# Optimization experiments

Hardware: AMD Instinct MI355X
Metric: run time of the kernel (lower is better)

Reference implementation:

```python
import jax, jax.numpy as jnp
import numpy as np

EPS = 1e-5
K = 3

def _bn(x, g, b):
    # training-mode BatchNorm2d: batch stats over (N,H,W), biased variance
    m = jnp.mean(x, axis=(0, 2, 3), keepdims=True)
    v = jnp.var(x, axis=(0, 2, 3), keepdims=True)
    return (x - m) * jax.lax.rsqrt(v + EPS) * g[None, :, None, None] + b[None, :, None, None]

def _gelu(x):
    return jax.nn.gelu(x, approximate=False)

def _dyn_dw(x, aw1, ab1, aw2, ab2):
    # dynamic depthwise conv: per-sample k^2 softmax weights shared over channels
    b, c, h, w = x.shape
    gap = jnp.mean(x, axis=(2, 3))                              # (b,c)
    h1 = jax.nn.relu(jnp.einsum('oc,bc->bo', aw1, gap) + ab1)   # (b,c//8)
    kw = jax.nn.softmax(jnp.einsum('oc,bc->bo', aw2, h1) + ab2, axis=1)  # (b,k^2)
    xp = jnp.pad(x, ((0, 0), (0, 0), (1, 1), (1, 1)))
    out = jnp.zeros_like(x)
    idx = 0
    for i in range(K):
        for j in range(K):
            out = out + kw[:, idx, None, None, None] * xp[:, :, i:i + h, j:j + w]
            idx += 1
    return out

def _channel_att(x, w1, w2):
    avg = jnp.mean(x, axis=(2, 3))        # (b,C)
    mx = jnp.max(x, axis=(2, 3))          # (b,C)
    def fc(v):
        return jnp.einsum('oc,bc->bo', w2, jax.nn.relu(jnp.einsum('oc,bc->bo', w1, v)))
    s = jax.nn.sigmoid(fc(avg) + fc(mx))  # (b,C)
    return s[:, :, None, None] * x

def _forward(x, w1, b1, g1, be1, aw1, ab1, aw2, ab2, g2, be2,
             ca_w1, ca_w2, pw, pb, g3, be3, sw, sb):
    b, n, d = x.shape
    h = w = int(np.sqrt(n))
    residual = x
    xi = jnp.transpose(x.reshape(b, h, w, d), (0, 3, 1, 2))       # (b,d,h,w)
    # pw_expand: 1x1 conv -> GELU -> BN
    y = jnp.einsum('oc,bchw->bohw', w1, xi) + b1[None, :, None, None]
    y = _bn(_gelu(y), g1, be1)                                    # (b,4d,h,w)
    # dw_conv: dynamic depthwise -> GELU -> BN -> channel attention
    y = _dyn_dw(y, aw1, ab1, aw2, ab2)
    y = _bn(_gelu(y), g2, be2)
    y = _channel_att(y, ca_w1, ca_w2)
    # spatial attention
    avg_o = jnp.mean(y, axis=1, keepdims=True)
    max_o = jnp.max(y, axis=1, keepdims=True)
    sp_in = jnp.concatenate([avg_o, max_o], axis=1)               # (b,2,h,w)
    sp = jax.lax.conv_general_dilated(sp_in, sw, (1, 1), ((3, 3), (3, 3)),
                                      dimension_numbers=('NCHW', 'OIHW', 'NCHW'))
    sp = jax.nn.sigmoid(sp + sb[None, :, None, None])
    y = y * sp
    # pw_project: 1x1 conv -> BN
    y = jnp.einsum('oc,bchw->bohw', pw, y) + pb[None, :, None, None]
    y = _bn(y, g3, be3)
    y = jnp.transpose(y, (0, 2, 3, 1)).reshape(b, n, d)
    return residual + y

def setup_inputs() -> dict:
    key = jax.random.key(0)
    ks = jax.random.split(key, 16)
    d, C = 256, 1024
    def rn(k, shape, fan):
        return jax.random.normal(k, shape, jnp.float32) * np.float32(np.sqrt(2.0 / fan))
    return {
        'x': jax.random.normal(ks[0], (8, 1024, d), jnp.float32),
        'w1': rn(ks[1], (C, d), d), 'b1': jnp.zeros((C,), jnp.float32),
        'g1': jnp.ones((C,), jnp.float32), 'be1': jnp.zeros((C,), jnp.float32),
        'aw1': rn(ks[2], (C // 8, C), C), 'ab1': jnp.zeros((C // 8,), jnp.float32),
        'aw2': rn(ks[3], (K * K, C // 8), C // 8), 'ab2': jnp.zeros((K * K,), jnp.float32),
        'g2': jnp.ones((C,), jnp.float32), 'be2': jnp.zeros((C,), jnp.float32),
        'ca_w1': rn(ks[4], (C // 16, C), C), 'ca_w2': rn(ks[5], (C, C // 16), C // 16),
        'pw': rn(ks[6], (d, C), C), 'pb': jnp.zeros((d,), jnp.float32),
        'g3': jnp.ones((d,), jnp.float32), 'be3': jnp.zeros((d,), jnp.float32),
        'sw': rn(ks[7], (1, 2, 7, 7), 2 * 49), 'sb': jnp.zeros((1,), jnp.float32),
    }

def reference(x, w1, b1, g1, be1, aw1, ab1, aw2, ab2, g2, be2,
              ca_w1, ca_w2, pw, pb, g3, be3, sw, sb):
    return _forward(x, w1, b1, g1, be1, aw1, ab1, aw2, ab2, g2, be2,
                    ca_w1, ca_w2, pw, pb, g3, be3, sw, sb)
```

## Files before the change

### kernel.cpp

```cpp
#include <hip/hip_runtime.h>
#include <math.h>

constexpr int B = 8;
constexpr int D = 256;
constexpr int C = 1024;
constexpr int H = 32, W = 32;
constexpr int P = H * W;
constexpr int M = B * P;
constexpr float EPS = 1e-5f;

typedef unsigned short u16;
typedef unsigned int u32;
typedef __attribute__((ext_vector_type(8))) short short8;
typedef __attribute__((ext_vector_type(4))) float floatx4;

constexpr size_t WS_CHSUM1 = 0;
constexpr size_t WS_CHSQ1  = 1024;
constexpr size_t WS_GAPSUM = 2048;
constexpr size_t WS_CHSUM3 = 10240;
constexpr size_t WS_CHSQ3  = 10496;
constexpr size_t WS_CHSUM2 = 10752;
constexpr size_t WS_CHSQ2  = 11776;
constexpr size_t WS_BSUM2  = 12800;
constexpr size_t WS_UMAX2  = 20992;
constexpr size_t WS_UMAXN2 = 29184;
constexpr size_t WS_ACC_COUNT = 37376;
constexpr size_t WS_SCALE1 = 37376;
constexpr size_t WS_SHIFT1 = 38400;
constexpr size_t WS_KW     = 39424;
constexpr size_t WS_SCALE2 = 39680;
constexpr size_t WS_SHIFT2 = 40704;
constexpr size_t WS_SATT   = 41728;
constexpr size_t WS_AVGO   = 49920;
constexpr size_t WS_MAXO   = 58112;
constexpr size_t WS_SP     = 66304;
constexpr size_t WS_PRE    = 74496;
constexpr size_t WS_T1B    = 2171648;
constexpr size_t WS_T2B    = 6365952;
constexpr size_t WS_XB     = 10560256;
constexpr size_t WS_W1B    = 11608832;
constexpr size_t WS_PWB    = 11739904;
constexpr size_t WS_YB     = 11870976;

__device__ __forceinline__ float gelu_exact(float v) {
    return 0.5f * v * (1.0f + erff(v * 0.70710678118654752440f));
}

__device__ __forceinline__ u16 f2bf(float f) {
    u32 u = __float_as_uint(f);
    u += 0x7fff + ((u >> 16) & 1);
    return (u16)(u >> 16);
}

__device__ __forceinline__ float bf2f(u16 v) {
    return __uint_as_float(((u32)v) << 16);
}

__device__ __forceinline__ u32 fkey(float f) {
    u32 u = __float_as_uint(f);
    return (u & 0x80000000u) ? ~u : (u | 0x80000000u);
}
__device__ __forceinline__ float fkeyinv(u32 k) {
    return __uint_as_float((k & 0x80000000u) ? (k ^ 0x80000000u) : ~k);
}

#define GLOAD(SRC, DST) __builtin_amdgcn_global_load_lds( \
    (const __attribute__((address_space(1))) void*)(SRC), \
    (__attribute__((address_space(3))) void*)(DST), 16, 0, 0)

__global__ __launch_bounds__(256) void cvt_all_kernel(const float* __restrict__ x,
                                                      const float* __restrict__ w1,
                                                      const float* __restrict__ pw,
                                                      u16* __restrict__ xb,
                                                      u16* __restrict__ w1b,
                                                      u16* __restrict__ pwb,
                                                      float* __restrict__ acc_zero) {
    const int i = blockIdx.x * 256 + threadIdx.x;
    if (i < (int)WS_ACC_COUNT) acc_zero[i] = 0.f;
    const float* src;
    u16* dst;
    int off;
    if (i < 524288)      { src = x;  dst = xb;  off = i; }
    else if (i < 589824) { src = w1; dst = w1b; off = i - 524288; }
    else                 { src = pw; dst = pwb; off = i - 589824; }
    const float4 v = *(const float4*)(src + (size_t)off * 4);
    uint2 o;
    o.x = ((u32)f2bf(v.x)) | ((u32)f2bf(v.y) << 16);
    o.y = ((u32)f2bf(v.z)) | ((u32)f2bf(v.w) << 16);
    *(uint2*)(dst + (size_t)off * 4) = o;
}

template<int KD, int EPI, int NS, int MB, int NB>
__global__ __launch_bounds__(256) void mfma_gemm_kernel(
    const u16* __restrict__ A,
    const u16* __restrict__ Bw,
    const float* __restrict__ bias,
    const float* __restrict__ rowscale,
    void* __restrict__ outv,
    float* __restrict__ csum,
    float* __restrict__ csq,
    float* __restrict__ gsum)
{
    constexpr int MI = MB / 32;
    constexpr int NJ = NB / 32;
    constexpr int ABUF = MB * 32;
    constexpr int BBUF = NB * 32;
    constexpr int BUFSZ = ABUF + BBUF;
    constexpr int GA = MB / 64;
    constexpr int GB = NB / 64;
    constexpr int LD = GA + GB;
    constexpr int NCH = KD / 32;
    constexpr int GX = NS / NB;
    constexpr int NWG = (M / MB) * GX;
    constexpr int CPX = NWG / 8;
    extern __shared__ u16 smem[];
    const int t = threadIdx.x;
    const int lane = t & 63;

    const int lin = blockIdx.y * GX + blockIdx.x;
    const int swz = (lin & 7) * CPX + (lin >> 3);
    const int bx = swz % GX;
    const int by = swz / GX;
    const int row0 = by * MB;
    const int col0 = bx * NB;

    const int wv = t >> 6;
    const int wrow = (wv >> 1) * (MB / 2);
    const int wcol = (wv & 1) * (NB / 2);
    const int lm = lane & 15;
    const int lk8 = (lane >> 4) * 8;
    const int srow = t >> 2;
    const int scol = (t & 3) * 8;
    const u16* gA = A + (size_t)(row0 + srow) * KD + scol;
    const u16* gB = Bw + (size_t)(col0 + srow) * KD + scol;

    const floatx4 zero = {0.f, 0.f, 0.f, 0.f};
    floatx4 acc[MI][NJ];
#pragma unroll
    for (int i = 0; i < MI; ++i)
#pragma unroll
        for (int j = 0; j < NJ; ++j) acc[i][j] = zero;

    auto stage = [&](u16* buf, int c) {
        const int kk = c * 32;
        u16* As = buf;
        u16* Bs = buf + ABUF;
#pragma unroll
        for (int g = 0; g < GA; ++g)
            GLOAD(gA + (size_t)g * 64 * KD + kk, As + g * 2048 + t * 8);
#pragma unroll
        for (int g = 0; g < GB; ++g)
            GLOAD(gB + (size_t)g * 64 * KD + kk, Bs + g * 2048 + t * 8);
    };
    auto compute = [&](const u16* buf) {
        const u16* As = buf;
        const u16* Bs = buf + ABUF;
        short8 af[MI], bf[NJ];
#pragma unroll
        for (int i = 0; i < MI; ++i)
            af[i] = *(const short8*)(As + (wrow + i * 16 + lm) * 32 + lk8);
#pragma unroll
        for (int j = 0; j < NJ; ++j)
            bf[j] = *(const short8*)(Bs + (wcol + j * 16 + lm) * 32 + lk8);
#pragma unroll
        for (int i = 0; i < MI; ++i)
#pragma unroll
            for (int j = 0; j < NJ; ++j)
                acc[i][j] = __builtin_amdgcn_mfma_f32_16x16x32_bf16(af[i], bf[j], acc[i][j], 0, 0, 0);
    };

    stage(smem, 0);
    for (int c = 0; c < NCH; ++c) {
        u16* curb = smem + (c & 1) * BUFSZ;
        if (c + 1 < NCH) {
            stage(smem + ((c + 1) & 1) * BUFSZ, c + 1);
            if constexpr (LD == 2) asm volatile("s_waitcnt vmcnt(2)" ::: "memory");
            else                   asm volatile("s_waitcnt vmcnt(3)" ::: "memory");
        } else {
            asm volatile("s_waitcnt vmcnt(0)" ::: "memory");
        }
        __builtin_amdgcn_s_barrier();
        compute(curb);
        asm volatile("s_waitcnt lgkmcnt(0)" ::: "memory");
        __builtin_amdgcn_s_barrier();
    }

    float colsum[NJ], colsq[NJ];
#pragma unroll
    for (int j = 0; j < NJ; ++j) { colsum[j] = 0.f; colsq[j] = 0.f; }

    if (EPI == 0) {
        u16* Cs = smem;
#pragma unroll
        for (int i = 0; i < MI; ++i) {
#pragma unroll
            for (int r = 0; r < 4; ++r) {
                const int lrow = wrow + i * 16 + (lane >> 4) * 4 + r;
#pragma unroll
                for (int j = 0; j < NJ; ++j) {
                    const int lcol = wcol + j * 16 + lm;
                    const float tv = gelu_exact(acc[i][j][r] + bias[col0 + lcol]);
                    Cs[lrow * NB + lcol] = f2bf(tv);
                    colsum[j] += tv;
                    colsq[j] = fmaf(tv, tv, colsq[j]);
                }
            }
        }
        __syncthreads();
        constexpr int TPR = NB / 8;
        constexpr int RPP = 256 / TPR;
        u16* outp = (u16*)outv;
#pragma unroll
        for (int p = 0; p < MB / RPP; ++p) {
            const int r = p * RPP + t / TPR;
            const int cc = (t % TPR) * 8;
            *(uint4*)(outp + (size_t)(row0 + r) * NS + col0 + cc) =
                *(const uint4*)(Cs + r * NB + cc);
        }
    } else {
        float* Cs = (float*)smem;
#pragma unroll
        for (int i = 0; i < MI; ++i) {
#pragma unroll
            for (int r = 0; r < 4; ++r) {
                const int lrow = wrow + i * 16 + (lane >> 4) * 4 + r;
                const float rs = rowscale[row0 + lrow];
#pragma unroll
                for (int j = 0; j < NJ; ++j) {
                    const int lcol = wcol + j * 16 + lm;
                    const float tv = rs * acc[i][j][r] + bias[col0 + lcol];
                    Cs[lrow * NB + lcol] = tv;
                    colsum[j] += tv;
                    colsq[j] = fmaf(tv, tv, colsq[j]);
                }
            }
        }
        __syncthreads();
        constexpr int TPR = NB / 4;
        constexpr int RPP = 256 / TPR;
        float* outp = (float*)outv;
#pragma unroll
        for (int p = 0; p < MB / RPP; ++p) {
            const int r = p * RPP + t / TPR;
            const int cc = (t % TPR) * 4;
            *(float4*)(outp + (size_t)(row0 + r) * NS + col0 + cc) =
                *(const float4*)(Cs + r * NB + cc);
        }
    }

    const int bb = (by * MB) >> 10;
#pragma unroll
    for (int j = 0; j < NJ; ++j) {
        float s = colsum[j];
        float q = colsq[j];
        s += __shfl_xor(s, 16); s += __shfl_xor(s, 32);
        q += __shfl_xor(q, 16); q += __shfl_xor(q, 32);
        if (lane < 16) {
            const int c = col0 + wcol + j * 16 + lm;
            atomicAdd(&csum[c], s);
            atomicAdd(&csq[c], q);
            if (EPI == 0) atomicAdd(&gsum[bb * NS + c], s);
        }
    }
}

__global__ __launch_bounds__(1024) void dynmlp_kernel(const float* __restrict__ chsum1,
                                                      const float* __restrict__ chsq1,
                                                      const float* __restrict__ gapsum,
                                                      const float* __restrict__ g1,
                                                      const float* __restrict__ be1,
                                                      const float* __restrict__ aw1,
                                                      const float* __restrict__ ab1,
                                                      const float* __restrict__ aw2,
                                                      const float* __restrict__ ab2,
                                                      float* __restrict__ scale1,
                                                      float* __restrict__ shift1,
                                                      float* __restrict__ kw) {
    const int b = blockIdx.x;
    const int t = threadIdx.x;
    const int wave = t >> 6, lane = t & 63;
    __shared__ float g[1024];
    __shared__ float h1[128];
    __shared__ float logits[12];
    {
        const float m = chsum1[t] * (1.0f / (float)M);
        const float var = chsq1[t] * (1.0f / (float)M) - m * m;
        const float rstd = rsqrtf(var + EPS);
        const float sc = rstd * g1[t];
        const float sh = be1[t] - m * sc;
        if (b == 0) { scale1[t] = sc; shift1[t] = sh; }
        g[t] = gapsum[b * C + t] * (1.0f / (float)P) * sc + sh;
    }
    __syncthreads();
#pragma unroll
    for (int k = 0; k < 8; ++k) {
        const int u = wave * 8 + k;
        const float4* wr = (const float4*)(aw1 + (size_t)u * C);
        float s = 0.f;
#pragma unroll
        for (int ch = 0; ch < 4; ++ch) {
            const float4 wv = wr[lane + 64 * ch];
            const float4 sv = *(const float4*)(g + 4 * lane + 256 * ch);
            s += wv.x * sv.x + wv.y * sv.y + wv.z * sv.z + wv.w * sv.w;
        }
#pragma unroll
        for (int off = 1; off < 64; off <<= 1) s += __shfl_xor(s, off);
        if (lane == 0) h1[u] = fmaxf(s + ab1[u], 0.f);
    }
    __syncthreads();
    if (wave < 9) {
        float s = aw2[wave * 128 + lane] * h1[lane]
                + aw2[wave * 128 + 64 + lane] * h1[64 + lane];
#pragma unroll
        for (int off = 1; off < 64; off <<= 1) s += __shfl_xor(s, off);
        if (lane == 0) logits[wave] = s + ab2[wave];
    }
    __syncthreads();
    if (t == 0) {
        float mx = logits[0];
        for (int i = 1; i < 9; ++i) mx = fmaxf(mx, logits[i]);
        float e[9], den = 0.f;
        for (int i = 0; i < 9; ++i) { e[i] = expf(logits[i] - mx); den += e[i]; }
        const float inv = 1.0f / den;
        for (int i = 0; i < 9; ++i) kw[b * 9 + i] = e[i] * inv;
    }
}

__global__ __launch_bounds__(256) void dwconv_kernel(const u16* __restrict__ t1b,
                                                     const float* __restrict__ scale1,
                                                     const float* __restrict__ shift1,
                                                     const float* __restrict__ kw,
                                                     u16* __restrict__ t2b,
                                                     float* __restrict__ chsum2,
                                                     float* __restrict__ chsq2,
                                                     float* __restrict__ bsum2,
                                                     u32* __restrict__ umax2,
                                                     u32* __restrict__ umaxn2) {
    __shared__ u16 rows[3 * 32 * 256];
    const int lin = blockIdx.y * 4 + blockIdx.x;
    const int swz = (lin & 7) * 128 + (lin >> 3);
    const int cq = swz & 3;
    const int bh = swz >> 2;
    const int b = bh >> 5;
    const int h = bh & 31;
    const int t = threadIdx.x;

    const u16* gbase = t1b + (size_t)b * P * C + cq * 256;
#pragma unroll
    for (int i = 0; i < 12; ++i) {
        const int lin2 = i * 256 + t;
        const int chunk = lin2 >> 5;
        const int r = chunk >> 5;
        const int w = chunk & 31;
        const int off8 = (lin2 & 31) * 8;
        const int hr = h + r - 1;
        uint4 v = {0u, 0u, 0u, 0u};
        if (hr >= 0 && hr < H)
            v = *(const uint4*)(gbase + (size_t)(hr * W + w) * C + off8);
        *(uint4*)(&rows[chunk * 256 + off8]) = v;
    }
    __syncthreads();

    const int c = t;
    const int gc = cq * 256 + c;
    float kk[9];
#pragma unroll
    for (int i = 0; i < 9; ++i) kk[i] = kw[b * 9 + i];
    const float sc = scale1[gc];
    const float sh = shift1[gc];
    float scm[3], shm[3];
    scm[0] = (h > 0)     ? sc : 0.f;  shm[0] = (h > 0)     ? sh : 0.f;
    scm[1] = sc;                      shm[1] = sh;
    scm[2] = (h < H - 1) ? sc : 0.f;  shm[2] = (h < H - 1) ? sh : 0.f;

    const u16* rp0 = rows + c;
#define DWVAL(ri, w) fmaf(bf2f(rp0[((ri) * 32 + (w)) * 256]), scm[ri], shm[ri])

    float vm0 = 0.f, vm1 = 0.f, vm2 = 0.f;
    float vc0 = DWVAL(0, 0), vc1 = DWVAL(1, 0), vc2 = DWVAL(2, 0);
    float vp0 = DWVAL(0, 1), vp1 = DWVAL(1, 1), vp2 = DWVAL(2, 1);

    float s = 0.f, q = 0.f, mx = -INFINITY, mn = INFINITY;
    u16* orow = t2b + ((size_t)b * P + h * W) * C + gc;
    for (int w = 0; w < W; ++w) {
        float acc;
        acc = kk[0] * vm0;
        acc = fmaf(kk[1], vc0, acc);
        acc = fmaf(kk[2], vp0, acc);
        acc = fmaf(kk[3], vm1, acc);
        acc = fmaf(kk[4], vc1, acc);
        acc = fmaf(kk[5], vp1, acc);
        acc = fmaf(kk[6], vm2, acc);
        acc = fmaf(kk[7], vc2, acc);
        acc = fmaf(kk[8], vp2, acc);
        const float y = gelu_exact(acc);
        orow[(size_t)w * C] = f2bf(y);
        s += y;
        q = fmaf(y, y, q);
        mx = fmaxf(mx, y);
        mn = fminf(mn, y);
        vm0 = vc0; vc0 = vp0;
        vm1 = vc1; vc1 = vp1;
        vm2 = vc2; vc2 = vp2;
        if (w + 2 < W) {
            vp0 = DWVAL(0, w + 2);
            vp1 = DWVAL(1, w + 2);
            vp2 = DWVAL(2, w + 2);
        } else {
            vp0 = 0.f; vp1 = 0.f; vp2 = 0.f;
        }
    }
#undef DWVAL
    atomicAdd(&chsum2[gc], s);
    atomicAdd(&chsq2[gc], q);
    atomicAdd(&bsum2[b * C + gc], s);
    atomicMax(&umax2[b * C + gc], fkey(mx));
    atomicMax(&umaxn2[b * C + gc], fkey(-mn));
}

__global__ __launch_bounds__(1024) void chatt_kernel(const float* __restrict__ chsum2,
                                                     const float* __restrict__ chsq2,
                                                     const float* __restrict__ bsum2,
                                                     const u32* __restrict__ umax2,
                                                     const u32* __restrict__ umaxn2,
                                                     const float* __restrict__ g2,
                                                     const float* __restrict__ be2,
                                                     const float* __restrict__ caw1,
                                                     const float* __restrict__ caw2,
                                                     float* __restrict__ scale2,
                                                     float* __restrict__ shift2,
                                                     float* __restrict__ s_att) {
    const int b = blockIdx.x;
    const int t = threadIdx.x;
    const int wave = t >> 6, lane = t & 63;
    __shared__ float la[1024], lx[1024], ha[64], hm[64];
    {
        const float m = chsum2[t] * (1.0f / (float)M);
        const float var = chsq2[t] * (1.0f / (float)M) - m * m;
        const float rstd = rsqrtf(var + EPS);
        const float sc = rstd * g2[t];
        const float sh = be2[t] - m * sc;
        if (b == 0) { scale2[t] = sc; shift2[t] = sh; }
        la[t] = bsum2[b * C + t] * (1.0f / (float)P) * sc + sh;
        const float mx = fkeyinv(umax2[b * C + t]);
        const float mn = -fkeyinv(umaxn2[b * C + t]);
        lx[t] = (sc >= 0.f ? mx : mn) * sc + sh;
    }
    __syncthreads();
#pragma unroll
    for (int k = 0; k < 8; ++k) {
        const int u = wave * 8 + k;
        const int row = u & 63;
        const float* src = (u < 64) ? la : lx;
        const float4* wr = (const float4*)(caw1 + (size_t)row * C);
        float s = 0.f;
#pragma unroll
        for (int ch = 0; ch < 4; ++ch) {
            const float4 wv = wr[lane + 64 * ch];
            const float4 sv = *(const float4*)(src + 4 * lane + 256 * ch);
            s += wv.x * sv.x + wv.y * sv.y + wv.z * sv.z + wv.w * sv.w;
        }
#pragma unroll
        for (int off = 1; off < 64; off <<= 1) s += __shfl_xor(s, off);
        if (lane == 0) {
            s = fmaxf(s, 0.f);
            if (u < 64) ha[row] = s; else hm[row] = s;
        }
    }
    __syncthreads();
    {
        const float4* w2 = (const float4*)(caw2 + (size_t)t * 64);
        float s = 0.f;
#pragma unroll
        for (int j = 0; j < 16; ++j) {
            const float4 wv = w2[j];
            s += wv.x * (ha[j * 4 + 0] + hm[j * 4 + 0]);
            s += wv.y * (ha[j * 4 + 1] + hm[j * 4 + 1]);
            s += wv.z * (ha[j * 4 + 2] + hm[j * 4 + 2]);
            s += wv.w * (ha[j * 4 + 3] + hm[j * 4 + 3]);
        }
        s_att[b * C + t] = 1.0f / (1.0f + expf(-s));
    }
}

__global__ __launch_bounds__(256) void yq_kernel(const u16* __restrict__ t2b,
                                                 const float* __restrict__ scale2,
                                                 const float* __restrict__ shift2,
                                                 const float* __restrict__ s_att,
                                                 u16* __restrict__ yb,
                                                 float* __restrict__ avg_o,
                                                 float* __restrict__ max_o) {
    const int row = blockIdx.x;
    const int b = row >> 10;
    const int t = threadIdx.x;
    const int c0 = t * 4;
    const uint2 vv = *(const uint2*)(t2b + (size_t)row * C + c0);
    const float v0 = bf2f((u16)(vv.x & 0xffff));
    const float v1 = bf2f((u16)(vv.x >> 16));
    const float v2 = bf2f((u16)(vv.y & 0xffff));
    const float v3 = bf2f((u16)(vv.y >> 16));
    const float4 sc = *(const float4*)(scale2 + c0);
    const float4 sh = *(const float4*)(shift2 + c0);
    const float4 sa = *(const float4*)(s_att + (size_t)b * C + c0);
    const float y0 = fmaf(v0, sc.x, sh.x) * sa.x;
    const float y1 = fmaf(v1, sc.y, sh.y) * sa.y;
    const float y2 = fmaf(v2, sc.z, sh.z) * sa.z;
    const float y3 = fmaf(v3, sc.w, sh.w) * sa.w;
    uint2 o;
    o.x = ((u32)f2bf(y0)) | ((u32)f2bf(y1) << 16);
    o.y = ((u32)f2bf(y2)) | ((u32)f2bf(y3) << 16);
    *(uint2*)(yb + (size_t)row * C + c0) = o;
    float s = (y0 + y1) + (y2 + y3);
    float mx = fmaxf(fmaxf(y0, y1), fmaxf(y2, y3));
#pragma unroll
    for (int off = 32; off > 0; off >>= 1) {
        s += __shfl_down(s, off);
        mx = fmaxf(mx, __shfl_down(mx, off));
    }
    __shared__ float ss[4], sm[4];
    const int wave = t >> 6, lane = t & 63;
    if (lane == 0) { ss[wave] = s; sm[wave] = mx; }
    __syncthreads();
    if (t == 0) {
        const float S = ss[0] + ss[1] + ss[2] + ss[3];
        const float Mx = fmaxf(fmaxf(sm[0], sm[1]), fmaxf(sm[2], sm[3]));
        avg_o[row] = S * (1.0f / (float)C);
        max_o[row] = Mx;
    }
}

__global__ __launch_bounds__(1024) void spconv_kernel(const float* __restrict__ avg_o,
                                                      const float* __restrict__ max_o,
                                                      const float* __restrict__ sw,
                                                      const float* __restrict__ sb,
                                                      float* __restrict__ sp) {
    const int b = blockIdx.x;
    const int t = threadIdx.x;
    __shared__ float pa[P], pm[P], wsh[98];
    pa[t] = avg_o[b * P + t];
    pm[t] = max_o[b * P + t];
    if (t < 98) wsh[t] = sw[t];
    const float sbv = sb[0];
    __syncthreads();
    const int h = t >> 5, w = t & 31;
    float acc = sbv;
#pragma unroll
    for (int i = 0; i < 7; ++i) {
        const int hh = h + i - 3;
        if (hh < 0 || hh >= H) continue;
#pragma unroll
        for (int j = 0; j < 7; ++j) {
            const int ww = w + j - 3;
            if (ww < 0 || ww >= W) continue;
            const int pidx = hh * W + ww;
            acc = fmaf(wsh[i * 7 + j], pa[pidx], acc);
            acc = fmaf(wsh[49 + i * 7 + j], pm[pidx], acc);
        }
    }
    sp[b * P + t] = 1.0f / (1.0f + expf(-acc));
}

__global__ __launch_bounds__(256) void final_kernel(const float* __restrict__ x,
                                                    const float* __restrict__ pre,
                                                    const float* __restrict__ chsum3,
                                                    const float* __restrict__ chsq3,
                                                    const float* __restrict__ g3,
                                                    const float* __restrict__ be3,
                                                    float* __restrict__ out) {
    __shared__ float lsc[256], lsh[256];
    const int t = threadIdx.x;
    {
        const float m = chsum3[t] * (1.0f / (float)M);
        const float var = chsq3[t] * (1.0f / (float)M) - m * m;
        const float rstd = rsqrtf(var + EPS);
        const float sc = rstd * g3[t];
        lsc[t] = sc;
        lsh[t] = be3[t] - m * sc;
    }
    __syncthreads();
    const int i = blockIdx.x * 256 + t;
    const int e = i * 4;
    const int d = e & 255;
    const float4 xv = *(const float4*)(x + e);
    const float4 pv = *(const float4*)(pre + e);
    const float4 sc = *(const float4*)(lsc + d);
    const float4 sh = *(const float4*)(lsh + d);
    float4 o;
    o.x = xv.x + fmaf(pv.x, sc.x, sh.x);
    o.y = xv.y + fmaf(pv.y, sc.y, sh.y);
    o.z = xv.z + fmaf(pv.z, sc.z, sh.z);
    o.w = xv.w + fmaf(pv.w, sc.w, sh.w);
    *(float4*)(out + e) = o;
}

extern "C" void kernel_launch(void* const* d_in, const int* in_sizes, int n_in,
                              void* d_out, int out_size, void* d_ws, size_t ws_size,
                              hipStream_t stream) {
    const float* x    = (const float*)d_in[0];
    const float* w1   = (const float*)d_in[1];
    const float* b1   = (const float*)d_in[2];
    const float* g1   = (const float*)d_in[3];
    const float* be1  = (const float*)d_in[4];
    const float* aw1  = (const float*)d_in[5];
    const float* ab1  = (const float*)d_in[6];
    const float* aw2  = (const float*)d_in[7];
    const float* ab2  = (const float*)d_in[8];
    const float* g2   = (const float*)d_in[9];
    const float* be2  = (const float*)d_in[10];
    const float* caw1 = (const float*)d_in[11];
    const float* caw2 = (const float*)d_in[12];
    const float* pw   = (const float*)d_in[13];
    const float* pb   = (const float*)d_in[14];
    const float* g3   = (const float*)d_in[15];
    const float* be3  = (const float*)d_in[16];
    const float* sw   = (const float*)d_in[17];
    const float* sb   = (const float*)d_in[18];
    float* out = (float*)d_out;
    float* ws = (float*)d_ws;

    float* chsum1  = ws + WS_CHSUM1;
    float* chsq1   = ws + WS_CHSQ1;
    float* gapsum  = ws + WS_GAPSUM;
    float* chsum3  = ws + WS_CHSUM3;
    float* chsq3   = ws + WS_CHSQ3;
    float* chsum2  = ws + WS_CHSUM2;
    float* chsq2   = ws + WS_CHSQ2;
    float* bsum2   = ws + WS_BSUM2;
    u32*   umax2   = (u32*)(ws + WS_UMAX2);
    u32*   umaxn2  = (u32*)(ws + WS_UMAXN2);
    float* scale1  = ws + WS_SCALE1;
    float* shift1  = ws + WS_SHIFT1;
    float* kw      = ws + WS_KW;
    float* scale2  = ws + WS_SCALE2;
    float* shift2  = ws + WS_SHIFT2;
    float* s_att   = ws + WS_SATT;
    float* avg_o   = ws + WS_AVGO;
    float* max_o   = ws + WS_MAXO;
    float* sp      = ws + WS_SP;
    float* pre     = ws + WS_PRE;
    u16* t1b = (u16*)(ws + WS_T1B);
    u16* t2b = (u16*)(ws + WS_T2B);
    u16* xb  = (u16*)(ws + WS_XB);
    u16* w1b = (u16*)(ws + WS_W1B);
    u16* pwb = (u16*)(ws + WS_PWB);
    u16* yb  = (u16*)(ws + WS_YB);

    cvt_all_kernel<<<dim3(2560), 256, 0, stream>>>(x, w1, pw, xb, w1b, pwb, ws);
    mfma_gemm_kernel<256, 0, C, 128, 64><<<dim3(C / 64, M / 128), 256, 24576, stream>>>(
        xb, w1b, b1, nullptr, t1b, chsum1, chsq1, gapsum);
    dynmlp_kernel<<<dim3(B), 1024, 0, stream>>>(chsum1, chsq1, gapsum, g1, be1,
                                                aw1, ab1, aw2, ab2, scale1, shift1, kw);
    dwconv_kernel<<<dim3(4, B * H), 256, 0, stream>>>(t1b, scale1, shift1, kw, t2b,
                                                      chsum2, chsq2, bsum2, umax2, umaxn2);
    chatt_kernel<<<dim3(B), 1024, 0, stream>>>(chsum2, chsq2, bsum2, umax2, umaxn2,
                                               g2, be2, caw1, caw2, scale2, shift2, s_att);
    yq_kernel<<<dim3(M), 256, 0, stream>>>(t2b, scale2, shift2, s_att, yb, avg_o, max_o);
    spconv_kernel<<<dim3(B), 1024, 0, stream>>>(avg_o, max_o, sw, sb, sp);
    mfma_gemm_kernel<1024, 1, D, 64, 64><<<dim3(D / 64, M / 64), 256, 16384, stream>>>(
        yb, pwb, pb, sp, pre, chsum3, chsq3, nullptr);
    final_kernel<<<dim3((M * D / 4) / 256), 256, 0, stream>>>(x, pre, chsum3, chsq3, g3, be3, out);
}
```

Baseline: 202.8 us.

## Fold BN2 and channel attention into per-batch projection weights, drop yb materialization

```diff
diff --git a/kernel.cpp b/kernel.cpp
--- a/kernel.cpp
+++ b/kernel.cpp
@@ -40,7 +40,8 @@
 constexpr size_t WS_XB     = 10560256;
 constexpr size_t WS_W1B    = 11608832;
 constexpr size_t WS_PWB    = 11739904;
-constexpr size_t WS_YB     = 11870976;
+constexpr size_t WS_PWBF   = 11870976;
+constexpr size_t WS_BIAS2  = 12919552;
 
 __device__ __forceinline__ float gelu_exact(float v) {
     return 0.5f * v * (1.0f + erff(v * 0.70710678118654752440f));
@@ -70,19 +71,16 @@
 
 __global__ __launch_bounds__(256) void cvt_all_kernel(const float* __restrict__ x,
                                                       const float* __restrict__ w1,
-                                                      const float* __restrict__ pw,
                                                       u16* __restrict__ xb,
                                                       u16* __restrict__ w1b,
-                                                      u16* __restrict__ pwb,
                                                       float* __restrict__ acc_zero) {
     const int i = blockIdx.x * 256 + threadIdx.x;
     if (i < (int)WS_ACC_COUNT) acc_zero[i] = 0.f;
     const float* src;
     u16* dst;
     int off;
-    if (i < 524288)      { src = x;  dst = xb;  off = i; }
-    else if (i < 589824) { src = w1; dst = w1b; off = i - 524288; }
-    else                 { src = pw; dst = pwb; off = i - 589824; }
+    if (i < 524288) { src = x;  dst = xb;  off = i; }
+    else            { src = w1; dst = w1b; off = i - 524288; }
     const float4 v = *(const float4*)(src + (size_t)off * 4);
     uint2 o;
     o.x = ((u32)f2bf(v.x)) | ((u32)f2bf(v.y) << 16);
@@ -123,6 +121,7 @@
     const int by = swz / GX;
     const int row0 = by * MB;
     const int col0 = bx * NB;
+    const int bb = row0 >> 10;
 
     const int wv = t >> 6;
     const int wrow = (wv >> 1) * (MB / 2);
@@ -132,7 +131,9 @@
     const int srow = t >> 2;
     const int scol = (t & 3) * 8;
     const u16* gA = A + (size_t)(row0 + srow) * KD + scol;
-    const u16* gB = Bw + (size_t)(col0 + srow) * KD + scol;
+    const u16* gB = Bw + (EPI == 1 ? (size_t)bb * NS * KD : (size_t)0)
+                       + (size_t)(col0 + srow) * KD + scol;
+    const float* biasp = bias + (EPI == 1 ? bb * NS : 0);
 
     const floatx4 zero = {0.f, 0.f, 0.f, 0.f};
     floatx4 acc[MI][NJ];
@@ -199,7 +200,7 @@
 #pragma unroll
                 for (int j = 0; j < NJ; ++j) {
                     const int lcol = wcol + j * 16 + lm;
-                    const float tv = gelu_exact(acc[i][j][r] + bias[col0 + lcol]);
+                    const float tv = gelu_exact(acc[i][j][r] + biasp[col0 + lcol]);
                     Cs[lrow * NB + lcol] = f2bf(tv);
                     colsum[j] += tv;
                     colsq[j] = fmaf(tv, tv, colsq[j]);
@@ -211,8 +212,8 @@
         constexpr int RPP = 256 / TPR;
         u16* outp = (u16*)outv;
 #pragma unroll
-        for (int p = 0; p < MB / RPP; ++p) {
-            const int r = p * RPP + t / TPR;
+        for (int pp = 0; pp < MB / RPP; ++pp) {
+            const int r = pp * RPP + t / TPR;
             const int cc = (t % TPR) * 8;
             *(uint4*)(outp + (size_t)(row0 + r) * NS + col0 + cc) =
                 *(const uint4*)(Cs + r * NB + cc);
@@ -228,7 +229,7 @@
 #pragma unroll
                 for (int j = 0; j < NJ; ++j) {
                     const int lcol = wcol + j * 16 + lm;
-                    const float tv = rs * acc[i][j][r] + bias[col0 + lcol];
+                    const float tv = rs * (acc[i][j][r] + biasp[col0 + lcol]);
                     Cs[lrow * NB + lcol] = tv;
                     colsum[j] += tv;
                     colsq[j] = fmaf(tv, tv, colsq[j]);
@@ -240,15 +241,14 @@
         constexpr int RPP = 256 / TPR;
         float* outp = (float*)outv;
 #pragma unroll
-        for (int p = 0; p < MB / RPP; ++p) {
-            const int r = p * RPP + t / TPR;
+        for (int pp = 0; pp < MB / RPP; ++pp) {
+            const int r = pp * RPP + t / TPR;
             const int cc = (t % TPR) * 4;
             *(float4*)(outp + (size_t)(row0 + r) * NS + col0 + cc) =
                 *(const float4*)(Cs + r * NB + cc);
         }
     }
 
-    const int bb = (by * MB) >> 10;
 #pragma unroll
     for (int j = 0; j < NJ; ++j) {
         float s = colsum[j];
@@ -427,19 +427,24 @@
                                                      const float* __restrict__ be2,
                                                      const float* __restrict__ caw1,
                                                      const float* __restrict__ caw2,
+                                                     const float* __restrict__ pw,
+                                                     const float* __restrict__ pb,
                                                      float* __restrict__ scale2,
                                                      float* __restrict__ shift2,
-                                                     float* __restrict__ s_att) {
+                                                     float* __restrict__ s_att,
+                                                     u16* __restrict__ pwb,
+                                                     float* __restrict__ bias2) {
     const int b = blockIdx.x;
     const int t = threadIdx.x;
     const int wave = t >> 6, lane = t & 63;
     __shared__ float la[1024], lx[1024], ha[64], hm[64];
+    float sc, sh;
     {
         const float m = chsum2[t] * (1.0f / (float)M);
         const float var = chsq2[t] * (1.0f / (float)M) - m * m;
         const float rstd = rsqrtf(var + EPS);
-        const float sc = rstd * g2[t];
-        const float sh = be2[t] - m * sc;
+        sc = rstd * g2[t];
+        sh = be2[t] - m * sc;
         if (b == 0) { scale2[t] = sc; shift2[t] = sh; }
         la[t] = bsum2[b * C + t] * (1.0f / (float)P) * sc + sh;
         const float mx = fkeyinv(umax2[b * C + t]);
@@ -468,6 +473,7 @@
         }
     }
     __syncthreads();
+    float sat;
     {
         const float4* w2 = (const float4*)(caw2 + (size_t)t * 64);
         float s = 0.f;
@@ -479,7 +485,32 @@
             s += wv.z * (ha[j * 4 + 2] + hm[j * 4 + 2]);
             s += wv.w * (ha[j * 4 + 3] + hm[j * 4 + 3]);
         }
-        s_att[b * C + t] = 1.0f / (1.0f + expf(-s));
+        sat = 1.0f / (1.0f + expf(-s));
+        s_att[b * C + t] = sat;
+    }
+    __syncthreads();
+    la[t] = sc * sat;
+    lx[t] = sh * sat;
+    __syncthreads();
+    {
+        const int d = t >> 2;
+        const int cbase = (t & 3) * 256;
+        const float* pwr = pw + (size_t)d * C + cbase;
+        u16* pwbr = pwb + ((size_t)b * D + d) * C + cbase;
+        float bacc = 0.f;
+        for (int i = 0; i < 256; i += 4) {
+            const float4 wv = *(const float4*)(pwr + i);
+            const float4 f1 = *(const float4*)(la + cbase + i);
+            const float4 f2 = *(const float4*)(lx + cbase + i);
+            uint2 o;
+            o.x = ((u32)f2bf(wv.x * f1.x)) | ((u32)f2bf(wv.y * f1.y) << 16);
+            o.y = ((u32)f2bf(wv.z * f1.z)) | ((u32)f2bf(wv.w * f1.w) << 16);
+            *(uint2*)(pwbr + i) = o;
+            bacc += wv.x * f2.x + wv.y * f2.y + wv.z * f2.z + wv.w * f2.w;
+        }
+        bacc += __shfl_xor(bacc, 1);
+        bacc += __shfl_xor(bacc, 2);
+        if ((t & 3) == 0) bias2[b * D + d] = pb[d] + bacc;
     }
 }
 
@@ -487,7 +518,6 @@
                                                  const float* __restrict__ scale2,
                                                  const float* __restrict__ shift2,
                                                  const float* __restrict__ s_att,
-                                                 u16* __restrict__ yb,
                                                  float* __restrict__ avg_o,
                                                  float* __restrict__ max_o) {
     const int row = blockIdx.x;
@@ -506,10 +536,6 @@
     const float y1 = fmaf(v1, sc.y, sh.y) * sa.y;
     const float y2 = fmaf(v2, sc.z, sh.z) * sa.z;
     const float y3 = fmaf(v3, sc.w, sh.w) * sa.w;
-    uint2 o;
-    o.x = ((u32)f2bf(y0)) | ((u32)f2bf(y1) << 16);
-    o.y = ((u32)f2bf(y2)) | ((u32)f2bf(y3) << 16);
-    *(uint2*)(yb + (size_t)row * C + c0) = o;
     float s = (y0 + y1) + (y2 + y3);
     float mx = fmaxf(fmaxf(y0, y1), fmaxf(y2, y3));
 #pragma unroll
@@ -638,14 +664,14 @@
     float* max_o   = ws + WS_MAXO;
     float* sp      = ws + WS_SP;
     float* pre     = ws + WS_PRE;
-    u16* t1b = (u16*)(ws + WS_T1B);
-    u16* t2b = (u16*)(ws + WS_T2B);
-    u16* xb  = (u16*)(ws + WS_XB);
-    u16* w1b = (u16*)(ws + WS_W1B);
-    u16* pwb = (u16*)(ws + WS_PWB);
-    u16* yb  = (u16*)(ws + WS_YB);
-
-    cvt_all_kernel<<<dim3(2560), 256, 0, stream>>>(x, w1, pw, xb, w1b, pwb, ws);
+    float* bias2   = ws + WS_BIAS2;
+    u16* t1b  = (u16*)(ws + WS_T1B);
+    u16* t2b  = (u16*)(ws + WS_T2B);
+    u16* xb   = (u16*)(ws + WS_XB);
+    u16* w1b  = (u16*)(ws + WS_W1B);
+    u16* pwbf = (u16*)(ws + WS_PWBF);
+
+    cvt_all_kernel<<<dim3(2304), 256, 0, stream>>>(x, w1, xb, w1b, ws);
     mfma_gemm_kernel<256, 0, C, 128, 64><<<dim3(C / 64, M / 128), 256, 24576, stream>>>(
         xb, w1b, b1, nullptr, t1b, chsum1, chsq1, gapsum);
     dynmlp_kernel<<<dim3(B), 1024, 0, stream>>>(chsum1, chsq1, gapsum, g1, be1,
@@ -653,10 +679,11 @@
     dwconv_kernel<<<dim3(4, B * H), 256, 0, stream>>>(t1b, scale1, shift1, kw, t2b,
                                                       chsum2, chsq2, bsum2, umax2, umaxn2);
     chatt_kernel<<<dim3(B), 1024, 0, stream>>>(chsum2, chsq2, bsum2, umax2, umaxn2,
-                                               g2, be2, caw1, caw2, scale2, shift2, s_att);
-    yq_kernel<<<dim3(M), 256, 0, stream>>>(t2b, scale2, shift2, s_att, yb, avg_o, max_o);
+                                               g2, be2, caw1, caw2, pw, pb,
+                                               scale2, shift2, s_att, pwbf, bias2);
+    yq_kernel<<<dim3(M), 256, 0, stream>>>(t2b, scale2, shift2, s_att, avg_o, max_o);
     spconv_kernel<<<dim3(B), 1024, 0, stream>>>(avg_o, max_o, sw, sb, sp);
-    mfma_gemm_kernel<1024, 1, D, 64, 64><<<dim3(D / 64, M / 64), 256, 16384, stream>>>(
-        yb, pwb, pb, sp, pre, chsum3, chsq3, nullptr);
+    mfma_gemm_kernel<1024, 1, D, 128, 64><<<dim3(D / 64, M / 128), 256, 32768, stream>>>(
+        t2b, pwbf, bias2, sp, pre, chsum3, chsq3, nullptr);
     final_kernel<<<dim3((M * D / 4) / 256), 256, 0, stream>>>(x, pre, chsum3, chsq3, g3, be3, out);
 }
```

Result: slower. 265.5 us (+30.9%).
